# Kernel tuning notes

Measured on AMD Instinct MI355X. Metric: run time of the kernel, lower is better.

## Reference

```python
import jax, jax.numpy as jnp
import numpy as np

B, S, HID = 2, 2048, 2048
NH = 16
HD = HID // NH  # 128


def setup_inputs() -> dict:
    key = jax.random.key(0)
    ks = jax.random.split(key, 12)
    sc = 0.02
    return {
        "hidden_state": jax.random.normal(ks[0], (B, S, HID), jnp.float32),
        "attention_mask": jax.random.uniform(ks[1], (B, 1, S, S), jnp.float32),
        "Wq": jax.random.normal(ks[2], (HID, HID), jnp.float32) * sc,
        "bq": jnp.zeros((HID,), jnp.float32),
        "Wk": jax.random.normal(ks[3], (HD, HID), jnp.float32) * sc,
        "bk": jnp.zeros((HD,), jnp.float32),
        "Wv": jax.random.normal(ks[4], (HD, HID), jnp.float32) * sc,
        "bv": jnp.zeros((HD,), jnp.float32),
        "Wo": jax.random.normal(ks[5], (HID, HID), jnp.float32) * sc,
        "bo": jnp.zeros((HID,), jnp.float32),
    }


def reference(hidden_state, attention_mask, Wq, bq, Wk, bk, Wv, bv, Wo, bo):
    b = hidden_state.shape[0]
    # projections (nn.Linear: x @ W.T + b)
    q = hidden_state @ Wq.T + bq                      # [B,S,HID]
    k = hidden_state @ Wk.T + bk                      # [B,S,HD] (single shared head)
    v = hidden_state @ Wv.T + bv                      # [B,S,HD]
    # split heads: q -> [B,NH,S,HD]
    q = q.reshape(b, -1, NH, HD).transpose(0, 2, 1, 3)
    scale = jnp.sqrt(jnp.asarray(HD, q.dtype))
    scores = jnp.einsum('bhsd,btd->bhst', q, k) / scale  # [B,NH,S,S]
    # faithful to source: mask scaled by -1e-09 (as written)
    scores = scores + attention_mask * (-1e-09)
    probs = jax.nn.softmax(scores, axis=-1)
    out = jnp.einsum('bhst,btd->bhsd', probs, v)          # [B,NH,S,HD]
    # faithful to source: transpose(-1,-2) then flat view to [B,S,HID]
    out = out.transpose(0, 1, 3, 2).reshape(b, -1, HD * NH)
    return out @ Wo.T + bo
```

## Files before the change

### kernel.cpp

```cpp
#include <hip/hip_runtime.h>
#include <hip/hip_bf16.h>

#define BATCH 2
#define SEQ 2048
#define HIDDIM 2048
#define NHEADS 16
#define HDIM 128
#define QKVN 2304

typedef __attribute__((ext_vector_type(8))) short bf16x8;
typedef __attribute__((ext_vector_type(4))) short short4v;
typedef __attribute__((ext_vector_type(4))) float f32x4;
typedef __attribute__((ext_vector_type(16))) float f32x16;
typedef __attribute__((ext_vector_type(4))) unsigned u32x4;

__device__ __forceinline__ short f2bf(float f) {
  unsigned u = __builtin_bit_cast(unsigned, f);
  unsigned r = (u + 0x7fffu + ((u >> 16) & 1u)) >> 16;
  return (short)r;
}

__device__ __forceinline__ unsigned cvtpk_bf16(float a, float b) {
  unsigned r;
  asm("v_cvt_pk_bf16_f32 %0, %1, %2" : "=v"(r) : "v"(a), "v"(b));
  return r;
}

#define PLSWAP(a, b) asm("v_permlane32_swap_b32 %0, %1" : "+v"(a), "+v"(b))

__device__ __forceinline__ void gl_lds16(const void* g, void* l) {
  __builtin_amdgcn_global_load_lds(
      (const __attribute__((address_space(1))) void*)g,
      (__attribute__((address_space(3))) void*)l, 16, 0, 0);
}

__device__ __forceinline__ float max3f(float a, float b, float c) {
  return fmaxf(fmaxf(a, b), c);
}
__device__ __forceinline__ float vmax16(const f32x16& v) {
  float a = max3f(v[0], v[1], v[2]);
  float b = max3f(v[3], v[4], v[5]);
  float c = max3f(v[6], v[7], v[8]);
  float d = max3f(v[9], v[10], v[11]);
  float e = max3f(v[12], v[13], v[14]);
  return fmaxf(max3f(a, b, c), max3f(d, e, v[15]));
}

__global__ void prep_kernel(const float* __restrict__ h, const float* __restrict__ Wq,
                            const float* __restrict__ Wk, const float* __restrict__ Wv,
                            const float* __restrict__ bq, const float* __restrict__ bk,
                            const float* __restrict__ bv,
                            short* __restrict__ h_bf, short* __restrict__ Wqkv_bf,
                            float* __restrict__ bqkv)
{
  int bid = blockIdx.x;
  const float* src;
  short* dst;
  int n;
  if (bid < 8192)        { src = h;  dst = h_bf;                n = 8388608; }
  else if (bid < 12288)  { src = Wq; dst = Wqkv_bf;             n = 4194304; bid -= 8192; }
  else if (bid < 12544)  { src = Wk; dst = Wqkv_bf + 4194304;   n = 262144;  bid -= 12288; }
  else if (bid < 12800)  { src = Wv; dst = Wqkv_bf + 4456448;   n = 262144;  bid -= 12544; }
  else {
    int i = (bid - 12800) * 256 + threadIdx.x;
    if (i < QKVN) {
      float v;
      if (i < HIDDIM) v = bq[i];
      else if (i < HIDDIM + HDIM) v = bk[i - HIDDIM];
      else v = bv[i - HIDDIM - HDIM];
      bqkv[i] = v;
    }
    return;
  }
  int i = (bid * 256 + threadIdx.x) * 4;
  if (i >= n) return;
  float4 v = *(const float4*)(src + i);
  short4v o;
  o[0] = f2bf(v.x); o[1] = f2bf(v.y); o[2] = f2bf(v.z); o[3] = f2bf(v.w);
  *(short4v*)(dst + i) = o;
}

__global__ void cvt_kernel(const float* __restrict__ in, short* __restrict__ out, int n) {
  int i = (blockIdx.x * blockDim.x + threadIdx.x) * 4;
  if (i >= n) return;
  float4 v = *(const float4*)(in + i);
  short4v o;
  o[0] = f2bf(v.x); o[1] = f2bf(v.y); o[2] = f2bf(v.z); o[3] = f2bf(v.w);
  *(short4v*)(out + i) = o;
}

template <int MODE>
__global__ __launch_bounds__(256, 2)
void gemm_bt(const short* __restrict__ A, const short* __restrict__ W,
             const float* __restrict__ bias, void* __restrict__ Cv, void* __restrict__ Cv2,
             int M, int N, int K, long sA, long sC)
{
  __shared__ short As[128 * 64];
  __shared__ short Ws[128 * 64];
  const int tid = threadIdx.x;
  const int lane = tid & 63;
  const int w = tid >> 6;
  const int wr = w >> 1, wc = w & 1;
  const int tm = blockIdx.y * 128, tn = blockIdx.x * 128;
  const short* Ap = A + (size_t)blockIdx.z * sA;

  const int rA = lane & 15;
  const int r7 = rA & 7;
  const int srow = lane >> 3;
  const int scg  = (lane & 7) ^ srow;

  f32x4 acc[4][4] = {};

  for (int k0 = 0; k0 < K; k0 += 64) {
    __syncthreads();
#pragma unroll
    for (int i = 0; i < 4; ++i) {
      int ch = w * 4 + i;
      gl_lds16(Ap + (size_t)(tm + ch * 8 + srow) * K + k0 + scg * 8, As + ch * 512);
      gl_lds16(W  + (size_t)(tn + ch * 8 + srow) * K + k0 + scg * 8, Ws + ch * 512);
    }
    __syncthreads();
#pragma unroll
    for (int kk = 0; kk < 64; kk += 32) {
      const int cg = (kk >> 3) + (lane >> 4);
      const int co = ((cg ^ r7) << 3);
      bf16x8 af[4];
#pragma unroll
      for (int mi = 0; mi < 4; ++mi)
        af[mi] = *(const bf16x8*)(As + ((wr * 64 + mi * 16 + rA) << 6) + co);
#pragma unroll
      for (int ni = 0; ni < 4; ++ni) {
        bf16x8 wf = *(const bf16x8*)(Ws + ((wc * 64 + ni * 16 + rA) << 6) + co);
#pragma unroll
        for (int mi = 0; mi < 4; ++mi)
          acc[mi][ni] = __builtin_amdgcn_mfma_f32_16x16x32_bf16(af[mi], wf, acc[mi][ni], 0, 0, 0);
      }
    }
  }

  const int cr = (lane >> 4) * 4;
  const int cc = lane & 15;
#pragma unroll
  for (int ni = 0; ni < 4; ++ni) {
    int col = tn + wc * 64 + ni * 16 + cc;
    float bv = bias[col];
#pragma unroll
    for (int mi = 0; mi < 4; ++mi) {
#pragma unroll
      for (int r = 0; r < 4; ++r) {
        int row = tm + wr * 64 + mi * 16 + cr + r;
        float v = acc[mi][ni][r] + bv;
        if constexpr (MODE == 0) {
          ((float*)Cv)[(size_t)blockIdx.z * sC + (size_t)row * N + col] = v;
        } else {
          if (col < HIDDIM + HDIM)
            ((short*)Cv)[(size_t)row * QKVN + col] = f2bf(v);
          else
            ((short*)Cv2)[(size_t)(col - HIDDIM - HDIM) * (BATCH * SEQ) + row] = f2bf(v);
        }
      }
    }
  }
}

__global__ __launch_bounds__(512, 2)
void attn_kernel(const short* __restrict__ QKV, const short* __restrict__ Vt,
                 short* __restrict__ OT)
{
  __shared__ short smem[2][32768];
  const int tid = threadIdx.x;
  const int l31 = tid & 31;
  const int hi2 = (tid >> 5) & 1;
  const int w = tid >> 6;
  const int b = blockIdx.z, h = blockIdx.y, qt = blockIdx.x;
  const float C2 = 0.12752600954427384f;
  const short* Kp = QKV + HIDDIM;

  const short* kptr[4];
  const short* vptr[4];
  {
    const int rin = (tid & 63) >> 4;
    const int gp = tid & 15;
#pragma unroll
    for (int i = 0; i < 4; ++i) {
      int ch = w * 4 + i;
      int row = ch * 4 + rin;
      int gl = gp ^ (row & 15);
      kptr[i] = Kp + (size_t)(b * SEQ + row) * QKVN + gl * 8;
      vptr[i] = Vt + (size_t)row * (BATCH * SEQ) + b * SEQ + gl * 8;
    }
  }

  bf16x8 qf[8];
  {
    const short* Qp = QKV + (size_t)(b * SEQ + qt * 256 + w * 32 + l31) * QKVN + h * HDIM;
#pragma unroll
    for (int kk = 0; kk < 8; ++kk)
      qf[kk] = *(const bf16x8*)(Qp + kk * 16 + hi2 * 8);
  }

  f32x16 o[4] = {};
  float m = -1e30f, l = 0.f;

#pragma unroll
  for (int i = 0; i < 4; ++i) {
    int ch = w * 4 + i;
    gl_lds16(kptr[i], (short*)smem[0] + ch * 512);
    gl_lds16(vptr[i], (short*)smem[0] + 16384 + ch * 512);
    kptr[i] += 128 * QKVN;
    vptr[i] += 128;
  }
  __syncthreads();

  for (int c = 0; c < 16; ++c) {
    const short* Ks = smem[c & 1];
    const short* Vs = smem[c & 1] + 16384;
    if (c < 15) {
      short* nb = smem[(c + 1) & 1];
#pragma unroll
      for (int i = 0; i < 4; ++i) {
        int ch = w * 4 + i;
        gl_lds16(kptr[i], nb + ch * 512);
        gl_lds16(vptr[i], nb + 16384 + ch * 512);
        kptr[i] += 128 * QKVN;
        vptr[i] += 128;
      }
    }

    f32x16 s[4] = {};
    __builtin_amdgcn_s_setprio(1);
#pragma unroll
    for (int n = 0; n < 4; ++n) {
      const int row = n * 32 + l31;
      const int rx = row & 15;
#pragma unroll
      for (int kk = 0; kk < 8; ++kk) {
        bf16x8 kf = *(const bf16x8*)(Ks + row * 128 + (((kk * 2 + hi2) ^ rx) << 3));
        s[n] = __builtin_amdgcn_mfma_f32_32x32x16_bf16(kf, qf[kk], s[n], 0, 0, 0);
      }
    }
    __builtin_amdgcn_s_setprio(0);

    float mx = fmaxf(fmaxf(vmax16(s[0]), vmax16(s[1])),
                     fmaxf(vmax16(s[2]), vmax16(s[3])));
    mx = fmaxf(mx, __shfl_xor(mx, 32));
    mx *= C2;
    if (!__all(mx <= m + 8.f)) {
      float mn = fmaxf(m, mx);
      float cf = exp2f(m - mn);
      m = mn; l *= cf;
#pragma unroll
      for (int nd = 0; nd < 4; ++nd)
#pragma unroll
        for (int r = 0; r < 16; ++r) o[nd][r] *= cf;
    }

    u32x4 pw[4][2];
    float rs = 0.f;
#pragma unroll
    for (int n = 0; n < 4; ++n) {
      float p[16];
#pragma unroll
      for (int r = 0; r < 16; ++r) {
        p[r] = exp2f(__builtin_fmaf(s[n][r], C2, -m));
        rs += p[r];
      }
      unsigned w0 = cvtpk_bf16(p[0], p[1]),  w1 = cvtpk_bf16(p[2], p[3]);
      unsigned w2 = cvtpk_bf16(p[4], p[5]),  w3 = cvtpk_bf16(p[6], p[7]);
      unsigned w4 = cvtpk_bf16(p[8], p[9]),  w5 = cvtpk_bf16(p[10], p[11]);
      unsigned w6 = cvtpk_bf16(p[12], p[13]), w7 = cvtpk_bf16(p[14], p[15]);
      PLSWAP(w0, w2); PLSWAP(w1, w3);
      PLSWAP(w4, w6); PLSWAP(w5, w7);
      pw[n][0] = (u32x4){w0, w1, w2, w3};
      pw[n][1] = (u32x4){w4, w5, w6, w7};
    }
    rs += __shfl_xor(rs, 32);
    l += rs;

    __builtin_amdgcn_s_setprio(1);
#pragma unroll
    for (int nd = 0; nd < 4; ++nd) {
      const int row = nd * 32 + l31;
      const int rx = row & 15;
#pragma unroll
      for (int n = 0; n < 4; ++n) {
#pragma unroll
        for (int t = 0; t < 2; ++t) {
          const int kvs = n * 2 + t;
          bf16x8 vf = *(const bf16x8*)(Vs + row * 128 + (((kvs * 2 + hi2) ^ rx) << 3));
          bf16x8 pa = __builtin_bit_cast(bf16x8, pw[n][t]);
          o[nd] = __builtin_amdgcn_mfma_f32_32x32x16_bf16(vf, pa, o[nd], 0, 0, 0);
        }
      }
    }
    __builtin_amdgcn_s_setprio(0);
    __syncthreads();
  }

  const float inv = 1.f / l;
  short* dst = OT + (size_t)b * (SEQ * HIDDIM) + (size_t)(h * HDIM) * SEQ
             + qt * 256 + w * 32 + l31;
#pragma unroll
  for (int nd = 0; nd < 4; ++nd) {
#pragma unroll
    for (int r = 0; r < 16; ++r) {
      int d = nd * 32 + (r & 3) + 8 * (r >> 2) + 4 * hi2;
      dst[(size_t)d * SEQ] = f2bf(o[nd][r] * inv);
    }
  }
}

extern "C" void kernel_launch(void* const* d_in, const int* in_sizes, int n_in,
                              void* d_out, int out_size, void* d_ws, size_t ws_size,
                              hipStream_t stream)
{
  const float* hidden = (const float*)d_in[0];
  const float* Wq = (const float*)d_in[2];
  const float* bq = (const float*)d_in[3];
  const float* Wk = (const float*)d_in[4];
  const float* bk = (const float*)d_in[5];
  const float* Wv = (const float*)d_in[6];
  const float* bv = (const float*)d_in[7];
  const float* Wo = (const float*)d_in[8];
  const float* bo = (const float*)d_in[9];
  float* out = (float*)d_out;

  short* ws      = (short*)d_ws;
  short* QKV     = ws;
  short* Wo_bf   = ws;
  short* Vt_bf   = ws + 9437184;
  short* h_bf    = Vt_bf + 524288;
  short* OT      = h_bf;
  short* Wqkv_bf = h_bf + 8388608;
  float* bqkv    = (float*)(Wqkv_bf + 4718592);

  prep_kernel<<<12809, 256, 0, stream>>>(hidden, Wq, Wk, Wv, bq, bk, bv,
                                         h_bf, Wqkv_bf, bqkv);

  gemm_bt<3><<<dim3(18, 32, 1), 256, 0, stream>>>(h_bf, Wqkv_bf, bqkv, QKV, Vt_bf,
                                                  4096, QKVN, 2048, 0, 0);
  attn_kernel<<<dim3(8, 16, 2), 512, 0, stream>>>(QKV, Vt_bf, OT);
  cvt_kernel<<<4096, 256, 0, stream>>>(Wo, Wo_bf, 4194304);
  gemm_bt<0><<<dim3(16, 16, 2), 256, 0, stream>>>(OT, Wo_bf, bo, out, nullptr,
                                                  2048, 2048, 2048, 4194304, 4194304);
}
```

Baseline: 197.3 us.

## Fold softmax scale into Q projection, interleave PV MFMAs, fuse Wo conversion

The QKV GEMM epilogue now multiplies Q by the softmax scale (with log2e) before rounding to bf16, so the attention kernel drops the per-element FMA and uses the raw hardware exp2. The P·V MFMAs are interleaved with the per-chunk exp/convert work instead of running after all probabilities are built, which lowers register pressure and overlaps math. When the workspace is large enough, the Wo fp32-to-bf16 conversion is merged into the prep kernel, removing one launch. Rounding scaled Q to bf16 and the approximate exp2 slightly change numerics.

```diff
diff --git a/kernel.cpp b/kernel.cpp
--- a/kernel.cpp
+++ b/kernel.cpp
@@ -48,10 +48,11 @@
 
 __global__ void prep_kernel(const float* __restrict__ h, const float* __restrict__ Wq,
                             const float* __restrict__ Wk, const float* __restrict__ Wv,
+                            const float* __restrict__ Wo,
                             const float* __restrict__ bq, const float* __restrict__ bk,
                             const float* __restrict__ bv,
                             short* __restrict__ h_bf, short* __restrict__ Wqkv_bf,
-                            float* __restrict__ bqkv)
+                            short* __restrict__ Wo_bf, float* __restrict__ bqkv)
 {
   int bid = blockIdx.x;
   const float* src;
@@ -61,7 +62,7 @@
   else if (bid < 12288)  { src = Wq; dst = Wqkv_bf;             n = 4194304; bid -= 8192; }
   else if (bid < 12544)  { src = Wk; dst = Wqkv_bf + 4194304;   n = 262144;  bid -= 12288; }
   else if (bid < 12800)  { src = Wv; dst = Wqkv_bf + 4456448;   n = 262144;  bid -= 12544; }
-  else {
+  else if (bid < 12809) {
     int i = (bid - 12800) * 256 + threadIdx.x;
     if (i < QKVN) {
       float v;
@@ -72,6 +73,7 @@
     }
     return;
   }
+  else                   { src = Wo; dst = Wo_bf;               n = 4194304; bid -= 12809; }
   int i = (bid * 256 + threadIdx.x) * 4;
   if (i >= n) return;
   float4 v = *(const float4*)(src + i);
@@ -138,6 +140,7 @@
     }
   }
 
+  const float QSCALE = 0.12752600954427384f;
   const int cr = (lane >> 4) * 4;
   const int cc = lane & 15;
 #pragma unroll
@@ -153,7 +156,9 @@
         if constexpr (MODE == 0) {
           ((float*)Cv)[(size_t)blockIdx.z * sC + (size_t)row * N + col] = v;
         } else {
-          if (col < HIDDIM + HDIM)
+          if (col < HIDDIM)
+            ((short*)Cv)[(size_t)row * QKVN + col] = f2bf(v * QSCALE);
+          else if (col < HIDDIM + HDIM)
             ((short*)Cv)[(size_t)row * QKVN + col] = f2bf(v);
           else
             ((short*)Cv2)[(size_t)(col - HIDDIM - HDIM) * (BATCH * SEQ) + row] = f2bf(v);
@@ -173,7 +178,7 @@
   const int hi2 = (tid >> 5) & 1;
   const int w = tid >> 6;
   const int b = blockIdx.z, h = blockIdx.y, qt = blockIdx.x;
-  const float C2 = 0.12752600954427384f;
+  const int rx = l31 & 15;
   const short* Kp = QKV + HIDDIM;
 
   const short* kptr[4];
@@ -232,7 +237,6 @@
 #pragma unroll
     for (int n = 0; n < 4; ++n) {
       const int row = n * 32 + l31;
-      const int rx = row & 15;
 #pragma unroll
       for (int kk = 0; kk < 8; ++kk) {
         bf16x8 kf = *(const bf16x8*)(Ks + row * 128 + (((kk * 2 + hi2) ^ rx) << 3));
@@ -244,10 +248,9 @@
     float mx = fmaxf(fmaxf(vmax16(s[0]), vmax16(s[1])),
                      fmaxf(vmax16(s[2]), vmax16(s[3])));
     mx = fmaxf(mx, __shfl_xor(mx, 32));
-    mx *= C2;
     if (!__all(mx <= m + 8.f)) {
       float mn = fmaxf(m, mx);
-      float cf = exp2f(m - mn);
+      float cf = __builtin_amdgcn_exp2f(m - mn);
       m = mn; l *= cf;
 #pragma unroll
       for (int nd = 0; nd < 4; ++nd)
@@ -255,45 +258,36 @@
         for (int r = 0; r < 16; ++r) o[nd][r] *= cf;
     }
 
-    u32x4 pw[4][2];
     float rs = 0.f;
 #pragma unroll
     for (int n = 0; n < 4; ++n) {
       float p[16];
 #pragma unroll
-      for (int r = 0; r < 16; ++r) {
-        p[r] = exp2f(__builtin_fmaf(s[n][r], C2, -m));
-        rs += p[r];
-      }
+      for (int r = 0; r < 16; ++r)
+        p[r] = __builtin_amdgcn_exp2f(s[n][r] - m);
+      rs += (((p[0] + p[1]) + (p[2] + p[3])) + ((p[4] + p[5]) + (p[6] + p[7])))
+          + (((p[8] + p[9]) + (p[10] + p[11])) + ((p[12] + p[13]) + (p[14] + p[15])));
       unsigned w0 = cvtpk_bf16(p[0], p[1]),  w1 = cvtpk_bf16(p[2], p[3]);
       unsigned w2 = cvtpk_bf16(p[4], p[5]),  w3 = cvtpk_bf16(p[6], p[7]);
       unsigned w4 = cvtpk_bf16(p[8], p[9]),  w5 = cvtpk_bf16(p[10], p[11]);
       unsigned w6 = cvtpk_bf16(p[12], p[13]), w7 = cvtpk_bf16(p[14], p[15]);
       PLSWAP(w0, w2); PLSWAP(w1, w3);
       PLSWAP(w4, w6); PLSWAP(w5, w7);
-      pw[n][0] = (u32x4){w0, w1, w2, w3};
-      pw[n][1] = (u32x4){w4, w5, w6, w7};
+      bf16x8 pa0 = __builtin_bit_cast(bf16x8, (u32x4){w0, w1, w2, w3});
+      bf16x8 pa1 = __builtin_bit_cast(bf16x8, (u32x4){w4, w5, w6, w7});
+      __builtin_amdgcn_s_setprio(1);
+#pragma unroll
+      for (int nd = 0; nd < 4; ++nd) {
+        const int row = nd * 32 + l31;
+        bf16x8 vf0 = *(const bf16x8*)(Vs + row * 128 + ((((n * 2) * 2 + hi2) ^ rx) << 3));
+        o[nd] = __builtin_amdgcn_mfma_f32_32x32x16_bf16(vf0, pa0, o[nd], 0, 0, 0);
+        bf16x8 vf1 = *(const bf16x8*)(Vs + row * 128 + ((((n * 2 + 1) * 2 + hi2) ^ rx) << 3));
+        o[nd] = __builtin_amdgcn_mfma_f32_32x32x16_bf16(vf1, pa1, o[nd], 0, 0, 0);
+      }
+      __builtin_amdgcn_s_setprio(0);
     }
     rs += __shfl_xor(rs, 32);
     l += rs;
-
-    __builtin_amdgcn_s_setprio(1);
-#pragma unroll
-    for (int nd = 0; nd < 4; ++nd) {
-      const int row = nd * 32 + l31;
-      const int rx = row & 15;
-#pragma unroll
-      for (int n = 0; n < 4; ++n) {
-#pragma unroll
-        for (int t = 0; t < 2; ++t) {
-          const int kvs = n * 2 + t;
-          bf16x8 vf = *(const bf16x8*)(Vs + row * 128 + (((kvs * 2 + hi2) ^ rx) << 3));
-          bf16x8 pa = __builtin_bit_cast(bf16x8, pw[n][t]);
-          o[nd] = __builtin_amdgcn_mfma_f32_32x32x16_bf16(vf, pa, o[nd], 0, 0, 0);
-        }
-      }
-    }
-    __builtin_amdgcn_s_setprio(0);
     __syncthreads();
   }
 
@@ -327,20 +321,23 @@
 
   short* ws      = (short*)d_ws;
   short* QKV     = ws;
-  short* Wo_bf   = ws;
   short* Vt_bf   = ws + 9437184;
   short* h_bf    = Vt_bf + 524288;
   short* OT      = h_bf;
   short* Wqkv_bf = h_bf + 8388608;
   float* bqkv    = (float*)(Wqkv_bf + 4718592);
-
-  prep_kernel<<<12809, 256, 0, stream>>>(hidden, Wq, Wk, Wv, bq, bk, bv,
-                                         h_bf, Wqkv_bf, bqkv);
+  short* Wo_sep  = (short*)(bqkv + QKVN);
+
+  const bool sep = ws_size >= (size_t)54535168;
+  short* Wo_bf = sep ? Wo_sep : QKV;
+
+  prep_kernel<<<sep ? 16905 : 12809, 256, 0, stream>>>(
+      hidden, Wq, Wk, Wv, Wo, bq, bk, bv, h_bf, Wqkv_bf, Wo_bf, bqkv);
 
   gemm_bt<3><<<dim3(18, 32, 1), 256, 0, stream>>>(h_bf, Wqkv_bf, bqkv, QKV, Vt_bf,
                                                   4096, QKVN, 2048, 0, 0);
   attn_kernel<<<dim3(8, 16, 2), 512, 0, stream>>>(QKV, Vt_bf, OT);
-  cvt_kernel<<<4096, 256, 0, stream>>>(Wo, Wo_bf, 4194304);
+  if (!sep) cvt_kernel<<<4096, 256, 0, stream>>>(Wo, Wo_bf, 4194304);
   gemm_bt<0><<<dim3(16, 16, 2), 256, 0, stream>>>(OT, Wo_bf, bo, out, nullptr,
                                                   2048, 2048, 2048, 4194304, 4194304);
 }
```

New measurement: 184.5 us. 6.5% less time.
